# Performance work log

Hardware: AMD Instinct MI355X
Metric: run time of the kernel (lower is better)

The kernel has to match this reference:

```python
import jax, jax.numpy as jnp
import numpy as np


def setup_inputs() -> dict:
    key = jax.random.key(0)
    ks = jax.random.split(key, 4)
    B, N, C, S, D_AGG, D_OUT = 16, 2048, 128, 25, 128, 128
    # sparse binary adjacency, avg degree ~ N*0.01 ~ 20
    A = (jax.random.uniform(ks[0], (B, N, N)) < 0.01).astype(jnp.float32)
    X = jax.random.normal(ks[1], (B, N, C), dtype=jnp.float32)
    Wa = jax.random.normal(ks[2], (C, D_AGG), dtype=jnp.float32) * 0.05
    ba = jnp.zeros((D_AGG,), jnp.float32)
    Wc = jax.random.normal(ks[3], (C + D_AGG, D_OUT), dtype=jnp.float32) * 0.05
    bc = jnp.zeros((D_OUT,), jnp.float32)
    return {"A": A, "X": X, "Wa": Wa, "ba": ba, "Wc": Wc, "bc": bc, "n_samples": S}


def reference(A, X, Wa, ba, Wc, bc, n_samples):
    # Per node: take up to n_samples neighbors (nonzero adjacency entries).
    # Original randomly subsamples when degree > S; we take the first S by
    # index (lax.top_k is stable, ties -> lowest index). Missing slots are
    # zero rows, matching the original tf.pad: they contribute relu(ba) to
    # the max-aggregator, exactly like the padded/no-neighbor branches.
    mask = (A != 0).astype(X.dtype)                      # [B,N,N]
    vals, idx = jax.lax.top_k(mask, n_samples)           # [B,N,S]
    feats = jax.vmap(lambda x, i: jnp.take(x, i, axis=0))(X, idx)  # [B,N,S,C]
    feats = feats * vals[..., None]                      # zero padded slots
    # max aggregator: relu(neigh @ Wa + ba), max over sampled neighbors
    h = jax.nn.relu(jnp.einsum('bnsc,cd->bnsd', feats, Wa) + ba)
    agg = h.max(axis=2)                                  # [B,N,D_AGG]
    # concat self features with aggregated, project, relu
    cat = jnp.concatenate([X, agg], axis=-1)             # [B,N,C+D_AGG]
    out = jax.nn.relu(jnp.einsum('bnk,ko->bno', cat, Wc) + bc)  # [B,N,D_OUT]
    # per-graph Frobenius-norm normalization with div_no_nan semantics
    norm = jnp.sqrt(jnp.sum(out * out, axis=(1, 2), keepdims=True))
    return jnp.where(norm > 0, out / norm, jnp.zeros_like(out))
```

## Files before the change

### kernel.cpp

```cpp
#include <hip/hip_runtime.h>


typedef __attribute__((ext_vector_type(8))) short short8;
typedef __attribute__((ext_vector_type(4))) float f32x4;
typedef __attribute__((ext_vector_type(4))) float fvec4;
typedef unsigned int uint;
typedef unsigned short ushort;

__device__ __forceinline__ ushort f2bf(float x) {
    uint u = __builtin_bit_cast(uint, x);
    u += 0x7FFFu + ((u >> 16) & 1u);
    return (ushort)(u >> 16);
}
__device__ __forceinline__ float bflo(uint h) { uint v = h << 16;         return __builtin_bit_cast(float, v); }
__device__ __forceinline__ float bfhi(uint h) { uint v = h & 0xFFFF0000u; return __builtin_bit_cast(float, v); }

__global__ __launch_bounds__(256) void gemm_k1_k(
    const float* __restrict__ X, const float* __restrict__ Wa,
    const float* __restrict__ ba, ushort* __restrict__ H)
{
    __shared__ ushort Asm[128 * 128];
    __shared__ ushort Bsm[128 * 128];
    const int tid = threadIdx.x, l = tid & 63, w = tid >> 6;
    const int wm = (w >> 1) * 64, wn = (w & 1) * 64;
    const size_t row0 = (size_t)blockIdx.x * 128;

#pragma unroll
    for (int j = 0; j < 8; ++j) {
        int gid = (j << 8) + tid;
        int r = gid >> 4, g = gid & 15;
        const float* s = X + (row0 + r) * 128 + g * 8;
        short8 pk;
#pragma unroll
        for (int e = 0; e < 8; ++e) pk[e] = (short)f2bf(s[e]);
        *(short8*)&Asm[r * 128 + ((g ^ (r & 7)) << 3)] = pk;
    }
    {
        int c = tid >> 1;
        int g0 = (tid & 1) * 8;
#pragma unroll
        for (int g = g0; g < g0 + 8; ++g) {
            short8 pk;
#pragma unroll
            for (int e = 0; e < 8; ++e)
                pk[e] = (short)f2bf(Wa[(size_t)(g * 8 + e) * 128 + c]);
            *(short8*)&Bsm[c * 128 + ((g ^ (c & 7)) << 3)] = pk;
        }
    }
    __syncthreads();

    f32x4 acc[4][4] = {};
#pragma unroll
    for (int ks = 0; ks < 4; ++ks) {
        int gg = (ks << 2) + (l >> 4);
        short8 af[4], bfr[4];
#pragma unroll
        for (int m = 0; m < 4; ++m) {
            int r = wm + m * 16 + (l & 15);
            af[m] = *(const short8*)&Asm[r * 128 + ((gg ^ (r & 7)) << 3)];
        }
#pragma unroll
        for (int n = 0; n < 4; ++n) {
            int c = wn + n * 16 + (l & 15);
            bfr[n] = *(const short8*)&Bsm[c * 128 + ((gg ^ (c & 7)) << 3)];
        }
#pragma unroll
        for (int m = 0; m < 4; ++m)
#pragma unroll
            for (int n = 0; n < 4; ++n)
                acc[m][n] = __builtin_amdgcn_mfma_f32_16x16x32_bf16(
                    af[m], bfr[n], acc[m][n], 0, 0, 0);
    }

    float bcol[4];
#pragma unroll
    for (int n = 0; n < 4; ++n) bcol[n] = ba[wn + n * 16 + (l & 15)];
#pragma unroll
    for (int m = 0; m < 4; ++m) {
        int rbase = wm + m * 16 + ((l >> 4) << 2);
#pragma unroll
        for (int n = 0; n < 4; ++n) {
            int col = wn + n * 16 + (l & 15);
#pragma unroll
            for (int r = 0; r < 4; ++r)
                H[(row0 + rbase + r) * 128 + col] =
                    f2bf(fmaxf(acc[m][n][r] + bcol[n], 0.f));
        }
    }
    if (blockIdx.x == 0 && tid < 64) {
        float a = fmaxf(ba[2 * tid], 0.f), b = fmaxf(ba[2 * tid + 1], 0.f);
        ((uint*)(H + (size_t)32768 * 128))[tid] =
            (uint)f2bf(a) | ((uint)f2bf(b) << 16);
    }
}

__global__ __launch_bounds__(256) void scan_k(
    const float* __restrict__ A,
    ushort* __restrict__ idxg,
    const int* __restrict__ nsp,
    const float* __restrict__ Wc,
    ushort* __restrict__ Wct,
    uint* __restrict__ ctr)
{
    if (blockIdx.x >= 8192) {
        int j = (blockIdx.x - 8192) * 256 + threadIdx.x;
        int d = j >> 8, k = j & 255;
        Wct[j] = f2bf(Wc[k * 128 + d]);
        if (blockIdx.x == 8192 && threadIdx.x == 0) *ctr = 0u;
        return;
    }

    __shared__ int idxs[4][32];
    const int l = threadIdx.x & 63;
    const int w = threadIdx.x >> 6;
    const int node = blockIdx.x * 4 + w;
    const int gbase = node & ~2047;
    int S = nsp[0]; if (S > 32) S = 32;

    const fvec4* rowp = (const fvec4*)(A + (size_t)node * 2048);
    fvec4 v[8];
#pragma unroll
    for (int c = 0; c < 8; ++c)
        v[c] = __builtin_nontemporal_load(rowp + c * 64 + l);

    const unsigned long long lt = (1ull << l) - 1ull;
    int base = 0;
#pragma unroll
    for (int c = 0; c < 8; ++c) {
        if (base < S) {
            unsigned long long m0 = __ballot(v[c][0] != 0.f);
            unsigned long long m1 = __ballot(v[c][1] != 0.f);
            unsigned long long m2 = __ballot(v[c][2] != 0.f);
            unsigned long long m3 = __ballot(v[c][3] != 0.f);
            int below = __popcll(m0 & lt) + __popcll(m1 & lt)
                      + __popcll(m2 & lt) + __popcll(m3 & lt);
            int o0 = (int)((m0 >> l) & 1), o1 = (int)((m1 >> l) & 1);
            int o2 = (int)((m2 >> l) & 1), o3 = (int)((m3 >> l) & 1);
            int r0 = base + below;
            int r1 = r0 + o0, r2 = r1 + o1, r3 = r2 + o2;
            int e = gbase + (c << 8) + (l << 2);
            if (o0 && r0 < S) idxs[w][r0] = e;
            if (o1 && r1 < S) idxs[w][r1] = e + 1;
            if (o2 && r2 < S) idxs[w][r2] = e + 2;
            if (o3 && r3 < S) idxs[w][r3] = e + 3;
            base += __popcll(m0) + __popcll(m1) + __popcll(m2) + __popcll(m3);
        }
    }
    int found = base < S ? base : S;
    int fill = (found > 0) ? idxs[w][0] : 32768;
    if (l < 32)
        idxg[(size_t)node * 32 + l] =
            (ushort)((l < found) ? idxs[w][l] : fill);
}

__global__ __launch_bounds__(256) void gather_k(
    const ushort* __restrict__ idxg,
    const uint*  __restrict__ Hu,
    const float* __restrict__ ba,
    uint* __restrict__ aggu)
{
    __shared__ ushort sidx[128];
    const int l = threadIdx.x & 63;
    const int w = threadIdx.x >> 6;
    const int bid = blockIdx.x, xcd = bid & 7, grp = bid >> 3;
    const int batch = ((grp >> 9) << 3) + xcd;
    const int node0 = (batch << 11) + ((grp & 511) << 2);
    const int node = node0 + w;

    if (threadIdx.x < 64)
        ((uint*)sidx)[threadIdx.x] =
            ((const uint*)(idxg + (size_t)node0 * 32))[threadIdx.x];
    __syncthreads();

    uint h[32];
#pragma unroll
    for (int q = 0; q < 32; ++q)
        h[q] = Hu[(size_t)sidx[w * 32 + q] * 64 + l];

    float i0 = fmaxf(ba[2 * l], 0.f), i1 = fmaxf(ba[2 * l + 1], 0.f);
    float a0[8], a1[8];
#pragma unroll
    for (int q = 0; q < 8; ++q) { a0[q] = i0; a1[q] = i1; }
#pragma unroll
    for (int q = 0; q < 32; ++q) {
        a0[q & 7] = fmaxf(a0[q & 7], bflo(h[q]));
        a1[q & 7] = fmaxf(a1[q & 7], bfhi(h[q]));
    }
#pragma unroll
    for (int q = 0; q < 4; ++q) {
        a0[q] = fmaxf(a0[q], a0[q + 4]);
        a1[q] = fmaxf(a1[q], a1[q + 4]);
    }
    float r0f = fmaxf(fmaxf(a0[0], a0[1]), fmaxf(a0[2], a0[3]));
    float r1f = fmaxf(fmaxf(a1[0], a1[1]), fmaxf(a1[2], a1[3]));
    aggu[(size_t)node * 64 + l] = (uint)f2bf(r0f) | ((uint)f2bf(r1f) << 16);
}

__global__ __launch_bounds__(256) void gemm_k3_k(
    const float* __restrict__ X, const ushort* __restrict__ agg,
    const ushort* __restrict__ Wct, const float* __restrict__ bc,
    float* __restrict__ out, float* __restrict__ partials,
    uint* __restrict__ ctr)
{
    __shared__ ushort Asm[128 * 128];
    __shared__ ushort Bsm[128 * 128];
    __shared__ float wred[4];
    __shared__ float ssc;
    const int tid = threadIdx.x, l = tid & 63, w = tid >> 6;
    const int wm = (w >> 1) * 64, wn = (w & 1) * 64;
    const int tile = blockIdx.x;
    const size_t row0 = (size_t)tile * 128;

    f32x4 acc[4][4] = {};
    for (int t = 0; t < 2; ++t) {
        __syncthreads();
        if (t == 0) {
#pragma unroll
            for (int j = 0; j < 8; ++j) {
                int gid = (j << 8) + tid;
                int r = gid >> 4, g = gid & 15;
                const float* s = X + (row0 + r) * 128 + g * 8;
                short8 pk;
#pragma unroll
                for (int e = 0; e < 8; ++e) pk[e] = (short)f2bf(s[e]);
                *(short8*)&Asm[r * 128 + ((g ^ (r & 7)) << 3)] = pk;
            }
        } else {
#pragma unroll
            for (int j = 0; j < 8; ++j) {
                int gid = (j << 8) + tid;
                int r = gid >> 4, g = gid & 15;
                short8 v = *(const short8*)(agg + (row0 + r) * 128 + g * 8);
                *(short8*)&Asm[r * 128 + ((g ^ (r & 7)) << 3)] = v;
            }
        }
#pragma unroll
        for (int j = 0; j < 8; ++j) {
            int gid = (j << 8) + tid;
            int r = gid >> 4, g = gid & 15;
            short8 v = *(const short8*)(Wct + (size_t)r * 256 + (t << 7) + g * 8);
            *(short8*)&Bsm[r * 128 + ((g ^ (r & 7)) << 3)] = v;
        }
        __syncthreads();
#pragma unroll
        for (int ks = 0; ks < 4; ++ks) {
            int gg = (ks << 2) + (l >> 4);
            short8 af[4], bfr[4];
#pragma unroll
            for (int m = 0; m < 4; ++m) {
                int r = wm + m * 16 + (l & 15);
                af[m] = *(const short8*)&Asm[r * 128 + ((gg ^ (r & 7)) << 3)];
            }
#pragma unroll
            for (int n = 0; n < 4; ++n) {
                int c = wn + n * 16 + (l & 15);
                bfr[n] = *(const short8*)&Bsm[c * 128 + ((gg ^ (c & 7)) << 3)];
            }
#pragma unroll
            for (int m = 0; m < 4; ++m)
#pragma unroll
                for (int n = 0; n < 4; ++n)
                    acc[m][n] = __builtin_amdgcn_mfma_f32_16x16x32_bf16(
                        af[m], bfr[n], acc[m][n], 0, 0, 0);
        }
    }

    float bcol[4];
#pragma unroll
    for (int n = 0; n < 4; ++n) bcol[n] = bc[wn + n * 16 + (l & 15)];
    float lsum = 0.f;
#pragma unroll
    for (int m = 0; m < 4; ++m)
#pragma unroll
        for (int n = 0; n < 4; ++n)
#pragma unroll
            for (int r = 0; r < 4; ++r) {
                float v = fmaxf(acc[m][n][r] + bcol[n], 0.f);
                acc[m][n][r] = v;
                lsum += v * v;
            }
#pragma unroll
    for (int off = 32; off > 0; off >>= 1) lsum += __shfl_down(lsum, off);
    if (l == 0) wred[w] = lsum;
    __syncthreads();
    if (tid == 0) {
        partials[tile] = wred[0] + wred[1] + wred[2] + wred[3];
        __threadfence();
        __hip_atomic_fetch_add(ctr, 1u, __ATOMIC_ACQ_REL,
                               __HIP_MEMORY_SCOPE_AGENT);
        while (__hip_atomic_load(ctr, __ATOMIC_ACQUIRE,
                                 __HIP_MEMORY_SCOPE_AGENT) < 256u)
            __builtin_amdgcn_s_sleep(8);
        float s = 0.f;
        const int bb = tile >> 4;
#pragma unroll
        for (int i = 0; i < 16; ++i)
            s += __hip_atomic_load(&partials[bb * 16 + i], __ATOMIC_RELAXED,
                                   __HIP_MEMORY_SCOPE_AGENT);
        float norm = sqrtf(s);
        ssc = (norm > 0.f) ? (1.f / norm) : 0.f;
    }
    __syncthreads();
    const float sc = ssc;
#pragma unroll
    for (int m = 0; m < 4; ++m) {
        int rbase = wm + m * 16 + ((l >> 4) << 2);
#pragma unroll
        for (int n = 0; n < 4; ++n) {
            int col = wn + n * 16 + (l & 15);
#pragma unroll
            for (int r = 0; r < 4; ++r)
                out[(row0 + rbase + r) * 128 + col] = acc[m][n][r] * sc;
        }
    }
}

extern "C" void kernel_launch(void* const* d_in, const int* in_sizes, int n_in,
                              void* d_out, int out_size, void* d_ws, size_t ws_size,
                              hipStream_t stream) {
    const float* A  = (const float*)d_in[0];
    const float* X  = (const float*)d_in[1];
    const float* Wa = (const float*)d_in[2];
    const float* ba = (const float*)d_in[3];
    const float* Wc = (const float*)d_in[4];
    const float* bc = (const float*)d_in[5];
    const int*  nsp = (const int*)d_in[6];

    float* out = (float*)d_out;
    char* ws = (char*)d_ws;
    ushort* H        = (ushort*)ws;
    ushort* agg      = (ushort*)(ws + (9u << 20));
    ushort* idxg     = (ushort*)(ws + (17u << 20));
    ushort* Wct      = (ushort*)(ws + (19u << 20));
    float*  partials = (float*) (ws + (19u << 20) + 65536);
    uint*   ctr      = (uint*)  (ws + (19u << 20) + 66560);

    gemm_k1_k<<<256, 256, 0, stream>>>(X, Wa, ba, H);
    scan_k<<<8192 + 128, 256, 0, stream>>>(A, idxg, nsp, Wc, Wct, ctr);
    gather_k<<<8192, 256, 0, stream>>>(idxg, (const uint*)H, ba, (uint*)agg);
    gemm_k3_k<<<256, 256, 0, stream>>>(X, agg, Wct, bc, out, partials, ctr);
}
```

Measured before the change: 96.33 us.

## Fuse neighbor scan with gather-max, replace grid spin barrier with scale kernel

```diff
diff --git a/kernel.cpp b/kernel.cpp
--- a/kernel.cpp
+++ b/kernel.cpp
@@ -14,6 +14,10 @@
 }
 __device__ __forceinline__ float bflo(uint h) { uint v = h << 16;         return __builtin_bit_cast(float, v); }
 __device__ __forceinline__ float bfhi(uint h) { uint v = h & 0xFFFF0000u; return __builtin_bit_cast(float, v); }
+__device__ __forceinline__ int mbcnt64(unsigned long long m) {
+    return __builtin_amdgcn_mbcnt_hi((uint)(m >> 32),
+           __builtin_amdgcn_mbcnt_lo((uint)m, 0u));
+}
 
 __global__ __launch_bounds__(256) void gemm_k1_k(
     const float* __restrict__ X, const float* __restrict__ Wa,
@@ -87,34 +91,32 @@
                     f2bf(fmaxf(acc[m][n][r] + bcol[n], 0.f));
         }
     }
-    if (blockIdx.x == 0 && tid < 64) {
-        float a = fmaxf(ba[2 * tid], 0.f), b = fmaxf(ba[2 * tid + 1], 0.f);
-        ((uint*)(H + (size_t)32768 * 128))[tid] =
-            (uint)f2bf(a) | ((uint)f2bf(b) << 16);
-    }
-}
-
-__global__ __launch_bounds__(256) void scan_k(
+}
+
+__global__ __launch_bounds__(256) void agg_k(
     const float* __restrict__ A,
-    ushort* __restrict__ idxg,
+    const uint*  __restrict__ Hu,
+    const float* __restrict__ ba,
+    uint* __restrict__ aggu,
     const int* __restrict__ nsp,
     const float* __restrict__ Wc,
-    ushort* __restrict__ Wct,
-    uint* __restrict__ ctr)
+    ushort* __restrict__ Wct)
 {
     if (blockIdx.x >= 8192) {
         int j = (blockIdx.x - 8192) * 256 + threadIdx.x;
         int d = j >> 8, k = j & 255;
         Wct[j] = f2bf(Wc[k * 128 + d]);
-        if (blockIdx.x == 8192 && threadIdx.x == 0) *ctr = 0u;
         return;
     }
 
     __shared__ int idxs[4][32];
     const int l = threadIdx.x & 63;
     const int w = threadIdx.x >> 6;
-    const int node = blockIdx.x * 4 + w;
-    const int gbase = node & ~2047;
+    const int bid   = blockIdx.x;
+    const int xcd   = bid & 7;
+    const int grp   = bid >> 3;
+    const int batch = ((grp >> 9) << 3) + xcd;
+    const int node  = (batch << 11) + ((grp & 511) << 2) + w;
     int S = nsp[0]; if (S > 32) S = 32;
 
     const fvec4* rowp = (const fvec4*)(A + (size_t)node * 2048);
@@ -123,7 +125,6 @@
     for (int c = 0; c < 8; ++c)
         v[c] = __builtin_nontemporal_load(rowp + c * 64 + l);
 
-    const unsigned long long lt = (1ull << l) - 1ull;
     int base = 0;
 #pragma unroll
     for (int c = 0; c < 8; ++c) {
@@ -132,13 +133,12 @@
             unsigned long long m1 = __ballot(v[c][1] != 0.f);
             unsigned long long m2 = __ballot(v[c][2] != 0.f);
             unsigned long long m3 = __ballot(v[c][3] != 0.f);
-            int below = __popcll(m0 & lt) + __popcll(m1 & lt)
-                      + __popcll(m2 & lt) + __popcll(m3 & lt);
+            int below = mbcnt64(m0) + mbcnt64(m1) + mbcnt64(m2) + mbcnt64(m3);
             int o0 = (int)((m0 >> l) & 1), o1 = (int)((m1 >> l) & 1);
             int o2 = (int)((m2 >> l) & 1), o3 = (int)((m3 >> l) & 1);
             int r0 = base + below;
             int r1 = r0 + o0, r2 = r1 + o1, r3 = r2 + o2;
-            int e = gbase + (c << 8) + (l << 2);
+            int e = (c << 8) + (l << 2);
             if (o0 && r0 < S) idxs[w][r0] = e;
             if (o1 && r1 < S) idxs[w][r1] = e + 1;
             if (o2 && r2 < S) idxs[w][r2] = e + 2;
@@ -147,69 +147,50 @@
         }
     }
     int found = base < S ? base : S;
-    int fill = (found > 0) ? idxs[w][0] : 32768;
-    if (l < 32)
-        idxg[(size_t)node * 32 + l] =
-            (ushort)((l < found) ? idxs[w][l] : fill);
-}
-
-__global__ __launch_bounds__(256) void gather_k(
-    const ushort* __restrict__ idxg,
-    const uint*  __restrict__ Hu,
-    const float* __restrict__ ba,
-    uint* __restrict__ aggu)
-{
-    __shared__ ushort sidx[128];
-    const int l = threadIdx.x & 63;
-    const int w = threadIdx.x >> 6;
-    const int bid = blockIdx.x, xcd = bid & 7, grp = bid >> 3;
-    const int batch = ((grp >> 9) << 3) + xcd;
-    const int node0 = (batch << 11) + ((grp & 511) << 2);
-    const int node = node0 + w;
-
-    if (threadIdx.x < 64)
-        ((uint*)sidx)[threadIdx.x] =
-            ((const uint*)(idxg + (size_t)node0 * 32))[threadIdx.x];
-    __syncthreads();
-
-    uint h[32];
-#pragma unroll
-    for (int q = 0; q < 32; ++q)
-        h[q] = Hu[(size_t)sidx[w * 32 + q] * 64 + l];
 
     float i0 = fmaxf(ba[2 * l], 0.f), i1 = fmaxf(ba[2 * l + 1], 0.f);
-    float a0[8], a1[8];
-#pragma unroll
-    for (int q = 0; q < 8; ++q) { a0[q] = i0; a1[q] = i1; }
-#pragma unroll
-    for (int q = 0; q < 32; ++q) {
-        a0[q & 7] = fmaxf(a0[q & 7], bflo(h[q]));
-        a1[q & 7] = fmaxf(a1[q & 7], bfhi(h[q]));
-    }
-#pragma unroll
-    for (int q = 0; q < 4; ++q) {
-        a0[q] = fmaxf(a0[q], a0[q + 4]);
-        a1[q] = fmaxf(a1[q], a1[q + 4]);
-    }
-    float r0f = fmaxf(fmaxf(a0[0], a0[1]), fmaxf(a0[2], a0[3]));
-    float r1f = fmaxf(fmaxf(a1[0], a1[1]), fmaxf(a1[2], a1[3]));
+    float r0f = i0, r1f = i1;
+    if (found > 0) {
+        int fill = idxs[w][0];
+        if (l < 32)
+            idxs[w][l] = (l < found) ? idxs[w][l] : fill;
+
+        const uint* HB = Hu + ((size_t)batch << 17);
+        uint h[32];
+#pragma unroll
+        for (int q = 0; q < 32; ++q)
+            h[q] = HB[(size_t)idxs[w][q] * 64 + l];
+
+        float a0[8], a1[8];
+#pragma unroll
+        for (int q = 0; q < 8; ++q) { a0[q] = i0; a1[q] = i1; }
+#pragma unroll
+        for (int q = 0; q < 32; ++q) {
+            a0[q & 7] = fmaxf(a0[q & 7], bflo(h[q]));
+            a1[q & 7] = fmaxf(a1[q & 7], bfhi(h[q]));
+        }
+#pragma unroll
+        for (int q = 0; q < 4; ++q) {
+            a0[q] = fmaxf(a0[q], a0[q + 4]);
+            a1[q] = fmaxf(a1[q], a1[q + 4]);
+        }
+        r0f = fmaxf(fmaxf(a0[0], a0[1]), fmaxf(a0[2], a0[3]));
+        r1f = fmaxf(fmaxf(a1[0], a1[1]), fmaxf(a1[2], a1[3]));
+    }
     aggu[(size_t)node * 64 + l] = (uint)f2bf(r0f) | ((uint)f2bf(r1f) << 16);
 }
 
 __global__ __launch_bounds__(256) void gemm_k3_k(
     const float* __restrict__ X, const ushort* __restrict__ agg,
     const ushort* __restrict__ Wct, const float* __restrict__ bc,
-    float* __restrict__ out, float* __restrict__ partials,
-    uint* __restrict__ ctr)
+    float* __restrict__ out, float* __restrict__ partials)
 {
     __shared__ ushort Asm[128 * 128];
     __shared__ ushort Bsm[128 * 128];
     __shared__ float wred[4];
-    __shared__ float ssc;
     const int tid = threadIdx.x, l = tid & 63, w = tid >> 6;
     const int wm = (w >> 1) * 64, wn = (w & 1) * 64;
-    const int tile = blockIdx.x;
-    const size_t row0 = (size_t)tile * 128;
+    const size_t row0 = (size_t)blockIdx.x * 128;
 
     f32x4 acc[4][4] = {};
     for (int t = 0; t < 2; ++t) {
@@ -270,48 +251,43 @@
     for (int n = 0; n < 4; ++n) bcol[n] = bc[wn + n * 16 + (l & 15)];
     float lsum = 0.f;
 #pragma unroll
-    for (int m = 0; m < 4; ++m)
-#pragma unroll
-        for (int n = 0; n < 4; ++n)
+    for (int m = 0; m < 4; ++m) {
+        int rbase = wm + m * 16 + ((l >> 4) << 2);
+#pragma unroll
+        for (int n = 0; n < 4; ++n) {
+            int col = wn + n * 16 + (l & 15);
 #pragma unroll
             for (int r = 0; r < 4; ++r) {
                 float v = fmaxf(acc[m][n][r] + bcol[n], 0.f);
-                acc[m][n][r] = v;
+                out[(row0 + rbase + r) * 128 + col] = v;
                 lsum += v * v;
             }
+        }
+    }
 #pragma unroll
     for (int off = 32; off > 0; off >>= 1) lsum += __shfl_down(lsum, off);
     if (l == 0) wred[w] = lsum;
     __syncthreads();
-    if (tid == 0) {
-        partials[tile] = wred[0] + wred[1] + wred[2] + wred[3];
-        __threadfence();
-        __hip_atomic_fetch_add(ctr, 1u, __ATOMIC_ACQ_REL,
-                               __HIP_MEMORY_SCOPE_AGENT);
-        while (__hip_atomic_load(ctr, __ATOMIC_ACQUIRE,
-                                 __HIP_MEMORY_SCOPE_AGENT) < 256u)
-            __builtin_amdgcn_s_sleep(8);
-        float s = 0.f;
-        const int bb = tile >> 4;
-#pragma unroll
-        for (int i = 0; i < 16; ++i)
-            s += __hip_atomic_load(&partials[bb * 16 + i], __ATOMIC_RELAXED,
-                                   __HIP_MEMORY_SCOPE_AGENT);
-        float norm = sqrtf(s);
-        ssc = (norm > 0.f) ? (1.f / norm) : 0.f;
-    }
-    __syncthreads();
-    const float sc = ssc;
-#pragma unroll
-    for (int m = 0; m < 4; ++m) {
-        int rbase = wm + m * 16 + ((l >> 4) << 2);
-#pragma unroll
-        for (int n = 0; n < 4; ++n) {
-            int col = wn + n * 16 + (l & 15);
-#pragma unroll
-            for (int r = 0; r < 4; ++r)
-                out[(row0 + rbase + r) * 128 + col] = acc[m][n][r] * sc;
-        }
+    if (tid == 0)
+        partials[blockIdx.x] = wred[0] + wred[1] + wred[2] + wred[3];
+}
+
+__global__ __launch_bounds__(256) void scale_k(
+    float* __restrict__ out, const float* __restrict__ partials)
+{
+    const int blk = blockIdx.x;
+    const int b = blk >> 6;
+    float s = 0.f;
+#pragma unroll
+    for (int i = 0; i < 16; ++i) s += partials[b * 16 + i];
+    float norm = sqrtf(s);
+    float sc = (norm > 0.f) ? (1.f / norm) : 0.f;
+    fvec4* o4 = (fvec4*)out;
+    int i0 = blk * 1024 + threadIdx.x;
+#pragma unroll
+    for (int k = 0; k < 4; ++k) {
+        fvec4 v = o4[i0 + k * 256];
+        o4[i0 + k * 256] = v * sc;
     }
 }
 
@@ -329,14 +305,13 @@
     float* out = (float*)d_out;
     char* ws = (char*)d_ws;
     ushort* H        = (ushort*)ws;
-    ushort* agg      = (ushort*)(ws + (9u << 20));
-    ushort* idxg     = (ushort*)(ws + (17u << 20));
-    ushort* Wct      = (ushort*)(ws + (19u << 20));
-    float*  partials = (float*) (ws + (19u << 20) + 65536);
-    uint*   ctr      = (uint*)  (ws + (19u << 20) + 66560);
+    ushort* agg      = (ushort*)(ws + (8u << 20));
+    ushort* Wct      = (ushort*)(ws + (16u << 20));
+    float*  partials = (float*) (ws + (16u << 20) + 65536);
 
     gemm_k1_k<<<256, 256, 0, stream>>>(X, Wa, ba, H);
-    scan_k<<<8192 + 128, 256, 0, stream>>>(A, idxg, nsp, Wc, Wct, ctr);
-    gather_k<<<8192, 256, 0, stream>>>(idxg, (const uint*)H, ba, (uint*)agg);
-    gemm_k3_k<<<256, 256, 0, stream>>>(X, agg, Wct, bc, out, partials, ctr);
-}
+    agg_k<<<8192 + 128, 256, 0, stream>>>(A, (const uint*)H, ba, (uint*)agg,
+                                          nsp, Wc, Wct);
+    gemm_k3_k<<<256, 256, 0, stream>>>(X, agg, Wct, bc, out, partials);
+    scale_k<<<1024, 256, 0, stream>>>(out, partials);
+}
```

Result: faster. 81.76 us (median of 2 runs) (-15.1%).
